# Kernel tuning notes

Hardware: AMD Instinct MI355X
Metric: run time of the kernel (lower is better)

The kernel has to match this reference:

```python
import jax, jax.numpy as jnp
import numpy as np

N, D, H, G = 4096, 256, 4, 16
HEAD_DIM = D // H
LN_EPS = 1e-5
TEMP = 5.0


def setup_inputs() -> dict:
    key = jax.random.key(0)
    ks = jax.random.split(key, 12)
    s = 0.05  # weight init scale
    nrm = lambda k, shp: jax.random.normal(k, shp, jnp.float32) * s
    return {
        "x": jax.random.normal(ks[0], (N, D), jnp.float32),
        "Wq": nrm(ks[1], (D, D)), "bq": jnp.zeros((D,), jnp.float32),
        "Wk": nrm(ks[2], (D, D)), "bk": jnp.zeros((D,), jnp.float32),
        "Wv": nrm(ks[3], (D, D)), "bv": jnp.zeros((D,), jnp.float32),
        "Wv1": nrm(ks[4], (D, D // 2)), "bv1": jnp.zeros((D // 2,), jnp.float32),
        "Wv2": nrm(ks[5], (D // 2, 1)), "bv2": jnp.zeros((1,), jnp.float32),
        "Wc1": nrm(ks[6], (2 * D, D)), "bc1": jnp.zeros((D,), jnp.float32),
        "Wc2": nrm(ks[7], (D, 1)), "bc2": jnp.zeros((1,), jnp.float32),
        "gamma": jnp.ones((D,), jnp.float32),
        "beta": jnp.zeros((D,), jnp.float32),
        "batch": jnp.sort(jax.random.randint(ks[8], (N,), 0, G)),
    }


def reference(x, Wq, bq, Wk, bk, Wv, bv, Wv1, bv1, Wv2, bv2,
              Wc1, bc1, Wc2, bc2, gamma, beta, batch):
    n = x.shape[0]
    # multi-head projections -> [N, H, head_dim]
    Q = (x @ Wq + bq).reshape(n, H, HEAD_DIM)
    K = (x @ Wk + bk).reshape(n, H, HEAD_DIM)
    V = (x @ Wv + bv).reshape(n, H, HEAD_DIM)

    # dense scores [N, N, H], block-diagonal mask by graph membership
    scores = jnp.einsum('nhd,mhd->nmh', Q, K) / np.sqrt(HEAD_DIM).astype(np.float32)
    same_graph = (batch[:, None] == batch[None, :])  # [N, N]
    scores = jnp.where(same_graph[:, :, None], scores, -jnp.inf)
    probs = jax.nn.softmax(scores, axis=1)  # softmax over keys m (dim=1, as in torch)
    # dropout is identity in eval mode
    attended = jnp.einsum('nmh,mhd->nhd', probs, V).reshape(n, D)

    # vulnerability detector MLP: D -> D/2 -> 1, sigmoid
    vuln = jax.nn.sigmoid(jax.nn.relu(x @ Wv1 + bv1) @ Wv2 + bv2)[:, 0]

    # global max pool per graph, broadcast back to nodes
    graph_ctx = jax.ops.segment_max(x, batch, num_segments=G, indices_are_sorted=True)[batch]
    combined = jnp.concatenate([x, graph_ctx], axis=1)  # [N, 2D]
    ctx = jax.nn.sigmoid(jnp.tanh(combined @ Wc1 + bc1) @ Wc2 + bc2)[:, 0]

    mha_avg = probs.mean(axis=(1, 2))  # [N]
    w = 0.6 * vuln + 0.3 * ctx + 0.1 * mha_avg

    # per-graph segment softmax with temperature 5.0
    w5 = w * TEMP
    seg_max = jax.ops.segment_max(w5, batch, num_segments=G, indices_are_sorted=True)[batch]
    e = jnp.exp(w5 - seg_max)
    seg_sum = jax.ops.segment_sum(e, batch, num_segments=G, indices_are_sorted=True)[batch]
    att = e / seg_sum  # [N]

    out = attended * att[:, None] + x  # residual
    # LayerNorm over last dim
    mu = out.mean(axis=-1, keepdims=True)
    var = out.var(axis=-1, keepdims=True)
    out = (out - mu) * jax.lax.rsqrt(var + LN_EPS) * gamma + beta
    return out, att
```

## Files before the change

### kernel.cpp

```cpp
#include <hip/hip_runtime.h>
#include <math.h>

#define N_NODES 4096
#define DIM 256
#define NH 4
#define NG 16
#define LN_EPS 1e-5f
#define TEMP 5.0f
#define RSLACK 4160
#define PS_STRIDE 72
#define BS_STRIDE 264
#define QP_MAX 12
#define K2_ATTN_BLOCKS (NG * QP_MAX)

typedef __attribute__((ext_vector_type(8))) short short8;
typedef __attribute__((ext_vector_type(4))) short short4_t;
typedef __attribute__((ext_vector_type(4))) float f32x4;

__device__ __forceinline__ unsigned short f2bf(float f) {
    unsigned u = __builtin_bit_cast(unsigned, f);
    u += 0x7FFFu + ((u >> 16) & 1u);
    return (unsigned short)(u >> 16);
}
__device__ __forceinline__ float bf2f(unsigned short u) {
    return __builtin_bit_cast(float, (unsigned)u << 16);
}
__device__ __forceinline__ float fsigmoid(float z) { return 1.f / (1.f + __expf(-z)); }
__device__ __forceinline__ float ftanh(float z) {
    float t = __expf(2.f * z);
    return (t - 1.f) / (t + 1.f);
}
__device__ __forceinline__ int seg_search(const int* __restrict__ batch, int g) {
    int lo = 0, hi = N_NODES;
    while (lo < hi) {
        int mid = (lo + hi) >> 1;
        if (batch[mid] < g) lo = mid + 1; else hi = mid;
    }
    return lo;
}

__device__ __forceinline__ short8 afrag_f32(const float* __restrict__ x, int row, int k0) {
    float4 a = *(const float4*)&x[(size_t)row * 256 + k0];
    float4 b = *(const float4*)&x[(size_t)row * 256 + k0 + 4];
    short8 r = {(short)f2bf(a.x), (short)f2bf(a.y), (short)f2bf(a.z), (short)f2bf(a.w),
                (short)f2bf(b.x), (short)f2bf(b.y), (short)f2bf(b.z), (short)f2bf(b.w)};
    return r;
}

__device__ __forceinline__ void ldsB(const float* __restrict__ W, int ws, int bn,
                                     unsigned short* __restrict__ Bs) {
    int c4 = (threadIdx.x & 15) * 4;
    int r0 = threadIdx.x >> 4;
    for (int p = 0; p < 16; ++p) {
        int k = p * 16 + r0;
        float4 wv = *(const float4*)&W[(size_t)k * ws + bn + c4];
        Bs[(c4 + 0) * BS_STRIDE + k] = f2bf(wv.x);
        Bs[(c4 + 1) * BS_STRIDE + k] = f2bf(wv.y);
        Bs[(c4 + 2) * BS_STRIDE + k] = f2bf(wv.z);
        Bs[(c4 + 3) * BS_STRIDE + k] = f2bf(wv.w);
    }
    __syncthreads();
}

__global__ __launch_bounds__(256) void k1_kernel(
    const float* __restrict__ x,
    const float* __restrict__ Wq, const float* __restrict__ bq,
    const float* __restrict__ Wk, const float* __restrict__ bk,
    const float* __restrict__ Wv, const float* __restrict__ bv,
    const float* __restrict__ Wv1, const float* __restrict__ bv1,
    const float* __restrict__ Wv2, const float* __restrict__ Wc1,
    const float* __restrict__ bc1, const int* __restrict__ batch,
    unsigned short* __restrict__ Qb, unsigned short* __restrict__ Kb,
    unsigned short* __restrict__ Vt, float* __restrict__ vacc2,
    float* __restrict__ Tpre, float* __restrict__ gcw, int* __restrict__ seg) {
    __shared__ __align__(16) char smem[64 * BS_STRIDE * 2];
    int id = blockIdx.x, tid = threadIdx.x;
    if (id < 16) {
        int g = id;
        int s = seg_search(batch, g), e = seg_search(batch, g + 1);
        float* red = (float*)smem;
        float* gl  = (float*)smem + 1024;
        int c4 = (tid & 63) * 4, way = tid >> 6;
        float4 mx = {-INFINITY, -INFINITY, -INFINITY, -INFINITY};
#pragma unroll 8
        for (int i = s + way; i < e; i += 4) {
            float4 v = *(const float4*)&x[(size_t)i * DIM + c4];
            mx.x = fmaxf(mx.x, v.x); mx.y = fmaxf(mx.y, v.y);
            mx.z = fmaxf(mx.z, v.z); mx.w = fmaxf(mx.w, v.w);
        }
        *(float4*)&red[way * 256 + c4] = mx;
        __syncthreads();
        if (way == 0) {
#pragma unroll
            for (int j = 0; j < 4; ++j) {
                float mm = fmaxf(fmaxf(red[c4 + j], red[256 + c4 + j]),
                                 fmaxf(red[512 + c4 + j], red[768 + c4 + j]));
                gl[c4 + j] = bf2f(f2bf(mm));
            }
        }
        __syncthreads();
        float ac[4] = {0.f, 0.f, 0.f, 0.f};
        for (int kb = 0; kb < 256; kb += 32) {
            float v[32];
#pragma unroll
            for (int j = 0; j < 32; ++j)
                v[j] = Wc1[(size_t)(256 + kb + j) * 256 + tid];
#pragma unroll
            for (int j = 0; j < 32; ++j) ac[j & 3] += gl[kb + j] * v[j];
        }
        gcw[g * 256 + tid] = (ac[0] + ac[1]) + (ac[2] + ac[3]);
        return;
    }
    if (id == 16) {
        if (tid <= NG) seg[tid] = seg_search(batch, tid);
        return;
    }
    int u = id - 17;
    unsigned short* Bs = (unsigned short*)smem;
    int w = tid >> 6, lane = tid & 63, m = lane & 15, quad = lane >> 4;
    if (u < 768) {
        int z = u >> 8, r = u & 255, bx = r & 63, by = r >> 6;
        const float* W = (z == 0) ? Wq : (z == 1) ? Wk : Wv;
        const float* bias = (z == 0) ? bq : (z == 1) ? bk : bv;
        ldsB(W, 256, by * 64, Bs);
        int rowA = bx * 64 + 16 * w + m;
        short8 a[8];
#pragma unroll
        for (int ks = 0; ks < 8; ++ks) a[ks] = afrag_f32(x, rowA, ks * 32 + quad * 8);
        int node0 = bx * 64 + 16 * w + quad * 4;
#pragma unroll
        for (int nt = 0; nt < 4; ++nt) {
            f32x4 acc = {0.f, 0.f, 0.f, 0.f};
#pragma unroll
            for (int ks = 0; ks < 8; ++ks) {
                short8 b = *(const short8*)&Bs[(nt * 16 + m) * BS_STRIDE + ks * 32 + quad * 8];
                acc = __builtin_amdgcn_mfma_f32_16x16x32_bf16(a[ks], b, acc, 0, 0, 0);
            }
            int col = by * 64 + nt * 16 + m;
            float bb = bias[col];
            if (z == 0) {
#pragma unroll
                for (int r2 = 0; r2 < 4; ++r2)
                    Qb[(size_t)(node0 + r2) * 256 + col] = f2bf((acc[r2] + bb) * 0.125f);
            } else if (z == 1) {
#pragma unroll
                for (int r2 = 0; r2 < 4; ++r2)
                    Kb[(size_t)(node0 + r2) * 256 + col] = f2bf(acc[r2] + bb);
            } else {
                short4_t pk = {(short)f2bf(acc[0] + bb), (short)f2bf(acc[1] + bb),
                               (short)f2bf(acc[2] + bb), (short)f2bf(acc[3] + bb)};
                *(short4_t*)&Vt[(size_t)col * RSLACK + node0] = pk;
            }
        }
    } else if (u < 896) {
        int r = u - 768, bx = r & 63, by = r >> 6;
        ldsB(Wv1, 128, by * 64, Bs);
        int rowA = bx * 64 + 16 * w + m;
        short8 a[8];
#pragma unroll
        for (int ks = 0; ks < 8; ++ks) a[ks] = afrag_f32(x, rowA, ks * 32 + quad * 8);
        int node0 = bx * 64 + 16 * w + quad * 4;
        float psum[4] = {0.f, 0.f, 0.f, 0.f};
#pragma unroll
        for (int nt = 0; nt < 4; ++nt) {
            f32x4 acc = {0.f, 0.f, 0.f, 0.f};
#pragma unroll
            for (int ks = 0; ks < 8; ++ks) {
                short8 b = *(const short8*)&Bs[(nt * 16 + m) * BS_STRIDE + ks * 32 + quad * 8];
                acc = __builtin_amdgcn_mfma_f32_16x16x32_bf16(a[ks], b, acc, 0, 0, 0);
            }
            int col = by * 64 + nt * 16 + m;
            float bb = bv1[col], wv = Wv2[col];
#pragma unroll
            for (int r2 = 0; r2 < 4; ++r2) psum[r2] += fmaxf(acc[r2] + bb, 0.f) * wv;
        }
#pragma unroll
        for (int r2 = 0; r2 < 4; ++r2) {
#pragma unroll
            for (int mm = 1; mm < 16; mm <<= 1) psum[r2] += __shfl_xor(psum[r2], mm);
            if (m == 0) vacc2[(size_t)(node0 + r2) * 2 + by] = psum[r2];
        }
    } else {
        int r = u - 896, bx = r & 63, by = r >> 6;
        ldsB(Wc1, 256, by * 64, Bs);
        int rowA = bx * 64 + 16 * w + m;
        short8 a[8];
#pragma unroll
        for (int ks = 0; ks < 8; ++ks) a[ks] = afrag_f32(x, rowA, ks * 32 + quad * 8);
        int node0 = bx * 64 + 16 * w + quad * 4;
#pragma unroll
        for (int nt = 0; nt < 4; ++nt) {
            f32x4 acc = {0.f, 0.f, 0.f, 0.f};
#pragma unroll
            for (int ks = 0; ks < 8; ++ks) {
                short8 b = *(const short8*)&Bs[(nt * 16 + m) * BS_STRIDE + ks * 32 + quad * 8];
                acc = __builtin_amdgcn_mfma_f32_16x16x32_bf16(a[ks], b, acc, 0, 0, 0);
            }
            int col = by * 64 + nt * 16 + m;
            float bb = bc1[col];
#pragma unroll
            for (int r2 = 0; r2 < 4; ++r2)
                Tpre[(size_t)(node0 + r2) * 256 + col] = acc[r2] + bb;
        }
    }
}

__global__ __launch_bounds__(256) void k2_kernel(
    const float* __restrict__ Tpre, const float* __restrict__ gcw,
    const float* __restrict__ Wc2, const int* __restrict__ batch,
    const unsigned short* __restrict__ Qb, const unsigned short* __restrict__ Kb,
    const unsigned short* __restrict__ Vt, const int* __restrict__ seg,
    unsigned short* __restrict__ Opart, float* __restrict__ Lpart,
    float* __restrict__ cacc) {
    __shared__ __align__(16) unsigned short Ks[64 * BS_STRIDE];
    __shared__ __align__(16) unsigned short Vs[256 * PS_STRIDE];
    __shared__ __align__(16) unsigned short Ps[4 * 16 * PS_STRIDE];
    int tid = threadIdx.x;
    if (blockIdx.x >= K2_ATTN_BLOCKS) {
        int id2 = blockIdx.x - K2_ATTN_BLOCKS;
        int nl = tid >> 4, cs = (tid & 15) * 16;
        int node = id2 * 16 + nl;
        int g = batch[node];
        float sum = 0.f;
#pragma unroll
        for (int j = 0; j < 16; ++j) {
            int c = cs + j;
            sum += ftanh(Tpre[(size_t)node * 256 + c] + gcw[g * 256 + c]) * Wc2[c];
        }
#pragma unroll
        for (int mm = 1; mm < 16; mm <<= 1) sum += __shfl_xor(sum, mm);
        if ((tid & 15) == 0) cacc[node] = sum;
        return;
    }
    int xw = blockIdx.x & 7, y = blockIdx.x >> 3;
    int g = xw * 2 + (y >= QP_MAX);
    int qp = (y >= QP_MAX) ? y - QP_MAX : y;
    int w = tid >> 6, lane = tid & 63, m = lane & 15, quad = lane >> 4;
    int h = w;
    int s = seg[g], e = seg[g + 1];
    int q0 = s + qp * 32;
    if (q0 >= e) return;

    short8 qa[2][2];
#pragma unroll
    for (int t = 0; t < 2; ++t) {
        qa[t][0] = *(const short8*)&Qb[(size_t)(q0 + t * 16 + m) * 256 + h * 64 + quad * 8];
        qa[t][1] = *(const short8*)&Qb[(size_t)(q0 + t * 16 + m) * 256 + h * 64 + 32 + quad * 8];
    }
    short8 ones = {16256, 16256, 16256, 16256, 16256, 16256, 16256, 16256};
    f32x4 O[2][4];
    f32x4 Lacc[2] = {{0.f, 0.f, 0.f, 0.f}, {0.f, 0.f, 0.f, 0.f}};
#pragma unroll
    for (int t = 0; t < 2; ++t)
#pragma unroll
        for (int nt = 0; nt < 4; ++nt) O[t][nt] = (f32x4){0.f, 0.f, 0.f, 0.f};
    int wbase = w * 16 * PS_STRIDE;
    int kr = tid >> 2, kc0 = (tid & 3) * 64;
    int voff = (tid & 7) * 8, vdr = tid >> 3;

    for (int kst = s; kst < e; kst += 64) {
        {
            const short8* ksrc = (const short8*)&Kb[(size_t)(kst + kr) * 256 + kc0];
            unsigned short* kdst = &Ks[kr * BS_STRIDE + kc0];
#pragma unroll
            for (int j = 0; j < 8; ++j) {
                int jj = (j + (tid & 3) * 2) & 7;
                *(short8*)&kdst[jj * 8] = ksrc[jj];
            }
        }
#pragma unroll
        for (int p = 0; p < 8; ++p) {
            int d = p * 32 + vdr;
            *(short8*)&Vs[d * PS_STRIDE + voff] =
                *(const short8*)&Vt[(size_t)d * RSLACK + kst + voff];
        }
        __syncthreads();
#pragma unroll
        for (int t = 0; t < 2; ++t) {
            if (q0 + t * 16 < e) {
                f32x4 S[4];
#pragma unroll
                for (int nt = 0; nt < 4; ++nt) {
                    short8 kf0 = *(const short8*)&Ks[(nt * 16 + m) * BS_STRIDE + h * 64 + quad * 8];
                    short8 kf1 = *(const short8*)&Ks[(nt * 16 + m) * BS_STRIDE + h * 64 + 32 + quad * 8];
                    f32x4 sa = {0.f, 0.f, 0.f, 0.f};
                    sa = __builtin_amdgcn_mfma_f32_16x16x32_bf16(qa[t][0], kf0, sa, 0, 0, 0);
                    sa = __builtin_amdgcn_mfma_f32_16x16x32_bf16(qa[t][1], kf1, sa, 0, 0, 0);
                    S[nt] = sa;
                }
                __builtin_amdgcn_wave_barrier();
#pragma unroll
                for (int nt = 0; nt < 4; ++nt) {
                    bool valid = (kst + nt * 16 + m) < e;
#pragma unroll
                    for (int r3 = 0; r3 < 4; ++r3) {
                        float p = valid ? __expf(S[nt][r3]) : 0.f;
                        Ps[wbase + (quad * 4 + r3) * PS_STRIDE + nt * 16 + m] = f2bf(p);
                    }
                }
                __builtin_amdgcn_wave_barrier();
                short8 pa0 = *(const short8*)&Ps[wbase + m * PS_STRIDE + quad * 8];
                short8 pa1 = *(const short8*)&Ps[wbase + m * PS_STRIDE + 32 + quad * 8];
                Lacc[t] = __builtin_amdgcn_mfma_f32_16x16x32_bf16(pa0, ones, Lacc[t], 0, 0, 0);
                Lacc[t] = __builtin_amdgcn_mfma_f32_16x16x32_bf16(pa1, ones, Lacc[t], 0, 0, 0);
#pragma unroll
                for (int nt = 0; nt < 4; ++nt) {
                    short8 vf0 = *(const short8*)&Vs[(h * 64 + nt * 16 + m) * PS_STRIDE + quad * 8];
                    short8 vf1 = *(const short8*)&Vs[(h * 64 + nt * 16 + m) * PS_STRIDE + 32 + quad * 8];
                    O[t][nt] = __builtin_amdgcn_mfma_f32_16x16x32_bf16(pa0, vf0, O[t][nt], 0, 0, 0);
                    O[t][nt] = __builtin_amdgcn_mfma_f32_16x16x32_bf16(pa1, vf1, O[t][nt], 0, 0, 0);
                }
            }
        }
        __syncthreads();
    }
#pragma unroll
    for (int t = 0; t < 2; ++t) {
#pragma unroll
        for (int r3 = 0; r3 < 4; ++r3) {
            int q = q0 + t * 16 + quad * 4 + r3;
            if (q < e) {
                if (m == 0) Lpart[(size_t)q * 4 + h] = Lacc[t][r3];
#pragma unroll
                for (int nt = 0; nt < 4; ++nt)
                    Opart[(size_t)q * 256 + h * 64 + nt * 16 + m] = f2bf(O[t][nt][r3]);
            }
        }
    }
}

__global__ __launch_bounds__(256) void k3_kernel(
    const unsigned short* __restrict__ Opart, const float* __restrict__ Lpart,
    const float* __restrict__ x, const float* __restrict__ vacc2,
    const float* __restrict__ cacc, const float* __restrict__ bv2,
    const float* __restrict__ bc2, const float* __restrict__ gamma,
    const float* __restrict__ beta, const int* __restrict__ batch,
    const int* __restrict__ seg, float* __restrict__ out,
    float* __restrict__ att_out) {
    __shared__ float wsc[776];
    __shared__ float gm[8], gsum[8];
    __shared__ float r1[4], r2[4];
    int tid = threadIdx.x;
    int n0 = blockIdx.x * 8;
    int gf = batch[n0], gl = batch[n0 + 7];
    int s0 = seg[gf], e1 = seg[gl + 1];
    float vb = bv2[0], cb = bc2[0];
    for (int j = s0 + tid; j < e1; j += 256) {
        float2 vv = *(const float2*)&vacc2[(size_t)j * 2];
        wsc[j - s0] = TEMP * (0.6f * fsigmoid(vv.x + vv.y + vb) +
                              0.3f * fsigmoid(cacc[j] + cb) + 0.1f / 4096.f);
    }
    __syncthreads();
    for (int g = gf; g <= gl; ++g) {
        int gs_ = seg[g], ge = seg[g + 1];
        float mx = -1e30f;
        for (int j = gs_ + tid; j < ge; j += 256) mx = fmaxf(mx, wsc[j - s0]);
#pragma unroll
        for (int k2 = 32; k2; k2 >>= 1) mx = fmaxf(mx, __shfl_xor(mx, k2));
        if ((tid & 63) == 0) r1[tid >> 6] = mx;
        __syncthreads();
        mx = fmaxf(fmaxf(r1[0], r1[1]), fmaxf(r1[2], r1[3]));
        float sm = 0.f;
        for (int j = gs_ + tid; j < ge; j += 256) sm += __expf(wsc[j - s0] - mx);
#pragma unroll
        for (int k2 = 32; k2; k2 >>= 1) sm += __shfl_xor(sm, k2);
        __syncthreads();
        if ((tid & 63) == 0) r2[tid >> 6] = sm;
        __syncthreads();
        if (tid == 0) {
            gm[g - gf] = mx;
            gsum[g - gf] = r2[0] + r2[1] + r2[2] + r2[3];
        }
        __syncthreads();
    }
    int h = tid >> 6;
    for (int i = 0; i < 8; ++i) {
        int n = n0 + i;
        int g = batch[n];
        float att_n = __expf(wsc[n - s0] - gm[g - gf]) / gsum[g - gf];
        if (tid == 0) att_out[n] = att_n;
        float L = Lpart[(size_t)n * 4 + h];
        float O = bf2f(Opart[(size_t)n * 256 + tid]);
        float o = (O / L) * att_n + x[(size_t)n * 256 + tid];
        float s1 = o, s2 = o * o;
#pragma unroll
        for (int k2 = 32; k2; k2 >>= 1) {
            s1 += __shfl_xor(s1, k2);
            s2 += __shfl_xor(s2, k2);
        }
        __syncthreads();
        if ((tid & 63) == 0) { r1[tid >> 6] = s1; r2[tid >> 6] = s2; }
        __syncthreads();
        float mu = (r1[0] + r1[1] + r1[2] + r1[3]) * (1.f / 256.f);
        float ms = (r2[0] + r2[1] + r2[2] + r2[3]) * (1.f / 256.f);
        float rs = rsqrtf(ms - mu * mu + LN_EPS);
        out[(size_t)n * 256 + tid] = (o - mu) * rs * gamma[tid] + beta[tid];
    }
}

extern "C" void kernel_launch(void* const* d_in, const int* in_sizes, int n_in,
                              void* d_out, int out_size, void* d_ws, size_t ws_size,
                              hipStream_t stream) {
    const float* x     = (const float*)d_in[0];
    const float* Wq    = (const float*)d_in[1];
    const float* bq    = (const float*)d_in[2];
    const float* Wk    = (const float*)d_in[3];
    const float* bk    = (const float*)d_in[4];
    const float* Wv    = (const float*)d_in[5];
    const float* bv    = (const float*)d_in[6];
    const float* Wv1   = (const float*)d_in[7];
    const float* bv1   = (const float*)d_in[8];
    const float* Wv2   = (const float*)d_in[9];
    const float* bv2   = (const float*)d_in[10];
    const float* Wc1   = (const float*)d_in[11];
    const float* bc1   = (const float*)d_in[12];
    const float* Wc2   = (const float*)d_in[13];
    const float* bc2   = (const float*)d_in[14];
    const float* gamma = (const float*)d_in[15];
    const float* beta  = (const float*)d_in[16];
    const int*   batch = (const int*)d_in[17];

    float* out = (float*)d_out;
    float* att = out + N_NODES * DIM;

    float* vacc2 = (float*)d_ws;
    float* cacc  = vacc2 + N_NODES * 2;
    float* gcw   = cacc + N_NODES;
    float* Lpart = gcw + NG * DIM;
    float* Tpre  = Lpart + N_NODES * 4;
    int*   seg   = (int*)(Tpre + N_NODES * DIM);
    unsigned short* Qb    = (unsigned short*)(seg + 32);
    unsigned short* Kb    = Qb + RSLACK * DIM;
    unsigned short* Vt    = Kb + RSLACK * DIM;
    unsigned short* Opart = Vt + DIM * RSLACK;

    k1_kernel<<<1169, 256, 0, stream>>>(x, Wq, bq, Wk, bk, Wv, bv, Wv1, bv1, Wv2,
                                        Wc1, bc1, batch, Qb, Kb, Vt, vacc2, Tpre,
                                        gcw, seg);
    k2_kernel<<<K2_ATTN_BLOCKS + 256, 256, 0, stream>>>(Tpre, gcw, Wc2, batch,
                                                        Qb, Kb, Vt, seg,
                                                        Opart, Lpart, cacc);
    k3_kernel<<<N_NODES / 8, 256, 0, stream>>>(Opart, Lpart, x, vacc2, cacc,
                                               bv2, bc2, gamma, beta, batch, seg,
                                               out, att);
}
```

Baseline: 141.1 us.

## Prefetch K/V tiles into registers, batch weight loads, wave-per-row LayerNorm

The attention kernel now loads the next K and V tile into registers while MFMA work runs on the current tile, then writes it to LDS after a barrier. This hides global-load latency at the cost of extra registers and an extra barrier per iteration. The weight staging helper issues eight float4 loads before converting and storing them, which raises memory-level parallelism. The final LayerNorm kernel now gives each wave two full rows with float4 loads and only shuffle reductions, removing the block-wide barriers it used per row.

```diff
diff --git a/kernel.cpp b/kernel.cpp
--- a/kernel.cpp
+++ b/kernel.cpp
@@ -51,13 +51,22 @@
                                      unsigned short* __restrict__ Bs) {
     int c4 = (threadIdx.x & 15) * 4;
     int r0 = threadIdx.x >> 4;
-    for (int p = 0; p < 16; ++p) {
-        int k = p * 16 + r0;
-        float4 wv = *(const float4*)&W[(size_t)k * ws + bn + c4];
-        Bs[(c4 + 0) * BS_STRIDE + k] = f2bf(wv.x);
-        Bs[(c4 + 1) * BS_STRIDE + k] = f2bf(wv.y);
-        Bs[(c4 + 2) * BS_STRIDE + k] = f2bf(wv.z);
-        Bs[(c4 + 3) * BS_STRIDE + k] = f2bf(wv.w);
+#pragma unroll
+    for (int hb = 0; hb < 2; ++hb) {
+        float4 wv[8];
+#pragma unroll
+        for (int p = 0; p < 8; ++p) {
+            int k = (hb * 8 + p) * 16 + r0;
+            wv[p] = *(const float4*)&W[(size_t)k * ws + bn + c4];
+        }
+#pragma unroll
+        for (int p = 0; p < 8; ++p) {
+            int k = (hb * 8 + p) * 16 + r0;
+            Bs[(c4 + 0) * BS_STRIDE + k] = f2bf(wv[p].x);
+            Bs[(c4 + 1) * BS_STRIDE + k] = f2bf(wv[p].y);
+            Bs[(c4 + 2) * BS_STRIDE + k] = f2bf(wv[p].z);
+            Bs[(c4 + 3) * BS_STRIDE + k] = f2bf(wv[p].w);
+        }
     }
     __syncthreads();
 }
@@ -258,23 +267,41 @@
     int kr = tid >> 2, kc0 = (tid & 3) * 64;
     int voff = (tid & 7) * 8, vdr = tid >> 3;
 
-    for (int kst = s; kst < e; kst += 64) {
-        {
-            const short8* ksrc = (const short8*)&Kb[(size_t)(kst + kr) * 256 + kc0];
-            unsigned short* kdst = &Ks[kr * BS_STRIDE + kc0];
-#pragma unroll
-            for (int j = 0; j < 8; ++j) {
-                int jj = (j + (tid & 3) * 2) & 7;
-                *(short8*)&kdst[jj * 8] = ksrc[jj];
-            }
-        }
+    short8 kpre[8], vpre[8];
+    {
+        const short8* ksrc = (const short8*)&Kb[(size_t)(s + kr) * 256 + kc0];
+#pragma unroll
+        for (int j = 0; j < 8; ++j) kpre[j] = ksrc[j];
 #pragma unroll
         for (int p = 0; p < 8; ++p) {
             int d = p * 32 + vdr;
-            *(short8*)&Vs[d * PS_STRIDE + voff] =
-                *(const short8*)&Vt[(size_t)d * RSLACK + kst + voff];
-        }
-        __syncthreads();
+            vpre[p] = *(const short8*)&Vt[(size_t)d * RSLACK + s + voff];
+        }
+    }
+    {
+        unsigned short* kdst = &Ks[kr * BS_STRIDE + kc0];
+#pragma unroll
+        for (int j = 0; j < 8; ++j) *(short8*)&kdst[j * 8] = kpre[j];
+#pragma unroll
+        for (int p = 0; p < 8; ++p) {
+            int d = p * 32 + vdr;
+            *(short8*)&Vs[d * PS_STRIDE + voff] = vpre[p];
+        }
+    }
+    __syncthreads();
+
+    for (int kst = s; kst < e; kst += 64) {
+        bool hasnext = (kst + 64) < e;
+        if (hasnext) {
+            const short8* ksrc = (const short8*)&Kb[(size_t)(kst + 64 + kr) * 256 + kc0];
+#pragma unroll
+            for (int j = 0; j < 8; ++j) kpre[j] = ksrc[j];
+#pragma unroll
+            for (int p = 0; p < 8; ++p) {
+                int d = p * 32 + vdr;
+                vpre[p] = *(const short8*)&Vt[(size_t)d * RSLACK + kst + 64 + voff];
+            }
+        }
 #pragma unroll
         for (int t = 0; t < 2; ++t) {
             if (q0 + t * 16 < e) {
@@ -312,7 +339,18 @@
                 }
             }
         }
-        __syncthreads();
+        if (hasnext) {
+            __syncthreads();
+            unsigned short* kdst = &Ks[kr * BS_STRIDE + kc0];
+#pragma unroll
+            for (int j = 0; j < 8; ++j) *(short8*)&kdst[j * 8] = kpre[j];
+#pragma unroll
+            for (int p = 0; p < 8; ++p) {
+                int d = p * 32 + vdr;
+                *(short8*)&Vs[d * PS_STRIDE + voff] = vpre[p];
+            }
+            __syncthreads();
+        }
     }
 #pragma unroll
     for (int t = 0; t < 2; ++t) {
@@ -373,28 +411,36 @@
         }
         __syncthreads();
     }
-    int h = tid >> 6;
-    for (int i = 0; i < 8; ++i) {
-        int n = n0 + i;
+    int w = tid >> 6, lane = tid & 63;
+    int c0 = lane * 4;
+#pragma unroll
+    for (int i = 0; i < 2; ++i) {
+        int n = n0 + w * 2 + i;
         int g = batch[n];
         float att_n = __expf(wsc[n - s0] - gm[g - gf]) / gsum[g - gf];
-        if (tid == 0) att_out[n] = att_n;
-        float L = Lpart[(size_t)n * 4 + h];
-        float O = bf2f(Opart[(size_t)n * 256 + tid]);
-        float o = (O / L) * att_n + x[(size_t)n * 256 + tid];
-        float s1 = o, s2 = o * o;
+        if (lane == 0) att_out[n] = att_n;
+        float L = Lpart[(size_t)n * 4 + (c0 >> 6)];
+        short4_t ov = *(const short4_t*)&Opart[(size_t)n * 256 + c0];
+        float4 xv = *(const float4*)&x[(size_t)n * 256 + c0];
+        float o0 = (bf2f((unsigned short)ov[0]) / L) * att_n + xv.x;
+        float o1 = (bf2f((unsigned short)ov[1]) / L) * att_n + xv.y;
+        float o2 = (bf2f((unsigned short)ov[2]) / L) * att_n + xv.z;
+        float o3 = (bf2f((unsigned short)ov[3]) / L) * att_n + xv.w;
+        float s1 = (o0 + o1) + (o2 + o3);
+        float s2 = (o0 * o0 + o1 * o1) + (o2 * o2 + o3 * o3);
 #pragma unroll
         for (int k2 = 32; k2; k2 >>= 1) {
             s1 += __shfl_xor(s1, k2);
             s2 += __shfl_xor(s2, k2);
         }
-        __syncthreads();
-        if ((tid & 63) == 0) { r1[tid >> 6] = s1; r2[tid >> 6] = s2; }
-        __syncthreads();
-        float mu = (r1[0] + r1[1] + r1[2] + r1[3]) * (1.f / 256.f);
-        float ms = (r2[0] + r2[1] + r2[2] + r2[3]) * (1.f / 256.f);
+        float mu = s1 * (1.f / 256.f);
+        float ms = s2 * (1.f / 256.f);
         float rs = rsqrtf(ms - mu * mu + LN_EPS);
-        out[(size_t)n * 256 + tid] = (o - mu) * rs * gamma[tid] + beta[tid];
+        float4 gv = *(const float4*)&gamma[c0];
+        float4 bvv = *(const float4*)&beta[c0];
+        float4 ov4 = {(o0 - mu) * rs * gv.x + bvv.x, (o1 - mu) * rs * gv.y + bvv.y,
+                      (o2 - mu) * rs * gv.z + bvv.z, (o3 - mu) * rs * gv.w + bvv.w};
+        *(float4*)&out[(size_t)n * 256 + c0] = ov4;
     }
 }
 
```

Measured after the change: 139.7 us. About the same (-1.0%).
